# Kernel tuning notes

Hardware: AMD Instinct MI355X
Metric: run time of the kernel (lower is better)

The kernel has to match this reference:

```python
import jax, jax.numpy as jnp
import numpy as np

SEQ = 256  # position axis length fixed by the graph's iota(256)


def _mod(freq, phase):
    # sin(2*pi*t*freq + phase)^2 * 0.1 + 1 - 0.05, shape [SEQ]
    t = jnp.arange(SEQ, dtype=jnp.float32)
    return jnp.sin(t * (2.0 * jnp.pi) * freq + phase) ** 2 * 0.1 + 0.95


def setup_inputs() -> dict:
    key = jax.random.key(0)
    ks = jax.random.split(key, 16)
    K = 2048  # number of scattered index triples
    return {
        "primals_1": jax.random.normal(ks[0], (6, 256, 256), jnp.float32),
        "primals_2": jax.random.normal(ks[1], (12, 6, 256), jnp.float32),
        "primals_3": jax.random.normal(ks[2], (6, 256, 256), jnp.float32),
        "primals_4": jax.random.normal(ks[3], (6, 256), jnp.float32),
        "primals_5": jax.random.randint(ks[4], (K,), 0, 6),
        "primals_6": jax.random.randint(ks[5], (K,), 0, 256),
        "primals_7": jax.random.randint(ks[6], (K,), 0, 256),
        "primals_8": jax.random.randint(ks[7], (K,), 0, 256),
        "primals_9": jax.random.uniform(ks[8], (1,), jnp.float32),
        "primals_10": jax.random.uniform(ks[9], (1,), jnp.float32),
        "primals_11": jax.random.normal(ks[10], (6, 256), jnp.float32),
        "primals_12": jax.random.uniform(ks[11], (1,), jnp.float32),
        "primals_13": jax.random.uniform(ks[12], (1,), jnp.float32),
        "primals_14": jax.random.normal(ks[13], (6, 256), jnp.float32),
        "primals_15": jax.random.uniform(ks[14], (1,), jnp.float32),
        "primals_16": jax.random.uniform(ks[15], (1,), jnp.float32),
    }


def reference(primals_1, primals_2, primals_3, primals_4, primals_5, primals_6,
              primals_7, primals_8, primals_9, primals_10, primals_11, primals_12,
              primals_13, primals_14, primals_15, primals_16):
    decay = primals_3 * 0.975  # reused in all three stages

    def stage(q, table, freq, phase):
        # gather from table [6,256] at (p5,p6) -> [K]
        vals = table[primals_5, primals_6]
        # scatter into a fresh copy of the persistent buffer, then decay-accumulate
        mem = primals_1.at[primals_5, primals_7, primals_8].set(vals) + decay  # [6,256,256]
        # bmm 'attention': q [12,6,256] x mem [6,256,256] -> [12,6,256]
        att = jnp.einsum('hbd,bde->hbe', q, mem)
        return att, _mod(freq, phase)

    a1, m1 = stage(primals_2, primals_4, primals_9, primals_10)
    x1 = a1 / m1
    a2, m2 = stage(x1, primals_11, primals_12, primals_13)
    x2 = a2 * m2
    a3, m3 = stage(x2, primals_14, primals_15, primals_16)
    return a3 / m3
```

## Files before the change

kernel.cpp:

```cpp
#include <hip/hip_runtime.h>

#define TWO_PI 6.2831853071795864769f

__global__ __launch_bounds__(1024, 4) void fused_chain(
    const float* __restrict__ P1, const float* __restrict__ P2,
    const float* __restrict__ P3, const float* __restrict__ T4,
    const int* __restrict__ p5, const int* __restrict__ p6,
    const int* __restrict__ p7, const int* __restrict__ p8,
    const float* __restrict__ f1, const float* __restrict__ ph1,
    const float* __restrict__ T11, const float* __restrict__ f2,
    const float* __restrict__ ph2, const float* __restrict__ T14,
    const float* __restrict__ f3, const float* __restrict__ ph3,
    float* __restrict__ out, int K)
{
    __shared__ float v[256];
    __shared__ float pv[16][256];
    __shared__ float modl[3][256];
    __shared__ unsigned hmap[4096];
    __shared__ unsigned short wde[2048];
    __shared__ float wv0[2048], wv1[2048], wv2[2048];
    __shared__ int nw;

    const int blk = blockIdx.x;
    const int h = blk / 6;
    const int b = blk - h * 6;
    const int tid = (int)threadIdx.x;
    const int dg = tid >> 6;
    const int eg = tid & 63;

    const float4* P1v = (const float4*)P1;
    const float4* P3v = (const float4*)P3;
    const int rbase = (b << 8) + (dg << 4);
    float4 m4[16];
    #pragma unroll
    for (int i = 0; i < 16; ++i) {
        float4 a = P1v[(rbase + i) * 64 + eg];
        float4 c = P3v[(rbase + i) * 64 + eg];
        m4[i].x = fmaf(c.x, 0.975f, a.x);
        m4[i].y = fmaf(c.y, 0.975f, a.y);
        m4[i].z = fmaf(c.z, 0.975f, a.z);
        m4[i].w = fmaf(c.w, 0.975f, a.w);
    }

    if (tid < 256) v[tid] = P2[(h * 6 + b) * 256 + tid];
    if (tid < 768) {
        int s = tid >> 8, ee = tid & 255;
        float fr = (s == 0) ? f1[0]  : (s == 1) ? f2[0]  : f3[0];
        float ph = (s == 0) ? ph1[0] : (s == 1) ? ph2[0] : ph3[0];
        float sn = sinf((float)ee * TWO_PI * fr + ph);
        float mm = sn * sn * 0.1f + 0.95f;
        modl[s][ee] = (s == 1) ? mm : 1.0f / mm;
    }
    for (int i = tid; i < 4096; i += 1024) hmap[i] = 0xFFFFFFFFu;
    if (tid == 0) nw = 0;
    __syncthreads();

    for (int k = tid; k < K; k += 1024) {
        if (p5[k] != b) continue;
        unsigned key = ((unsigned)p7[k] << 8) | (unsigned)p8[k];
        unsigned mine = (key << 12) | (unsigned)k;
        unsigned hh = (key * 2654435761u) >> 20;
        for (;;) {
            unsigned prev = atomicCAS(&hmap[hh], 0xFFFFFFFFu, mine);
            if (prev == 0xFFFFFFFFu) break;
            if ((prev >> 12) == key) { atomicMax(&hmap[hh], mine); break; }
            hh = (hh + 1) & 4095u;
        }
    }
    __syncthreads();

    for (int k = tid; k < K; k += 1024) {
        if (p5[k] != b) continue;
        unsigned key = ((unsigned)p7[k] << 8) | (unsigned)p8[k];
        unsigned hh = (key * 2654435761u) >> 20;
        unsigned cur;
        for (;;) {
            cur = hmap[hh];
            if ((cur >> 12) == key) break;
            hh = (hh + 1) & 4095u;
        }
        if ((cur & 0xFFFu) == (unsigned)k) {
            int c = p6[k];
            float p1v = P1[(b << 16) | key];
            int w = atomicAdd(&nw, 1);
            wde[w] = (unsigned short)key;
            wv0[w] = T4 [b * 256 + c] - p1v;
            wv1[w] = T11[b * 256 + c] - p1v;
            wv2[w] = T14[b * 256 + c] - p1v;
        }
    }
    __syncthreads();
    const int nwl = nw;

    const int e256 = tid & 255;
    for (int s = 0; s < 3; ++s) {
        float4 acc = make_float4(0.f, 0.f, 0.f, 0.f);
        #pragma unroll
        for (int j = 0; j < 4; ++j) {
            float4 vv = *(const float4*)&v[(dg << 4) + (j << 2)];
            float4 m0 = m4[(j << 2) + 0];
            float4 m1 = m4[(j << 2) + 1];
            float4 m2 = m4[(j << 2) + 2];
            float4 m3 = m4[(j << 2) + 3];
            acc.x = fmaf(vv.x, m0.x, acc.x); acc.y = fmaf(vv.x, m0.y, acc.y);
            acc.z = fmaf(vv.x, m0.z, acc.z); acc.w = fmaf(vv.x, m0.w, acc.w);
            acc.x = fmaf(vv.y, m1.x, acc.x); acc.y = fmaf(vv.y, m1.y, acc.y);
            acc.z = fmaf(vv.y, m1.z, acc.z); acc.w = fmaf(vv.y, m1.w, acc.w);
            acc.x = fmaf(vv.z, m2.x, acc.x); acc.y = fmaf(vv.z, m2.y, acc.y);
            acc.z = fmaf(vv.z, m2.z, acc.z); acc.w = fmaf(vv.z, m2.w, acc.w);
            acc.x = fmaf(vv.w, m3.x, acc.x); acc.y = fmaf(vv.w, m3.y, acc.y);
            acc.z = fmaf(vv.w, m3.z, acc.z); acc.w = fmaf(vv.w, m3.w, acc.w);
        }
        *(float4*)&pv[dg][eg << 2] = acc;
        __syncthreads();
        {
            int r = tid >> 8;
            float x = pv[r][e256] + pv[r + 4][e256] +
                      pv[r + 8][e256] + pv[r + 12][e256];
            __syncthreads();
            pv[r][e256] = x;
        }
        __syncthreads();
        if (tid < 256)
            pv[0][tid] = (pv[0][tid] + pv[1][tid]) + (pv[2][tid] + pv[3][tid]);
        __syncthreads();
        const float* wvs = (s == 0) ? wv0 : (s == 1) ? wv1 : wv2;
        for (int i = tid; i < nwl; i += 1024) {
            unsigned de = wde[i];
            atomicAdd(&pv[0][de & 255u], v[de >> 8] * wvs[i]);
        }
        __syncthreads();
        if (tid < 256)
            v[tid] = pv[0][tid] * modl[s][tid];
        __syncthreads();
    }
    if (tid < 256) out[(h * 6 + b) * 256 + tid] = v[tid];
}

extern "C" void kernel_launch(void* const* d_in, const int* in_sizes, int n_in,
                              void* d_out, int out_size, void* d_ws, size_t ws_size,
                              hipStream_t stream)
{
    (void)n_in; (void)out_size; (void)d_ws; (void)ws_size;
    const float* P1  = (const float*)d_in[0];
    const float* P2  = (const float*)d_in[1];
    const float* P3  = (const float*)d_in[2];
    const float* T4  = (const float*)d_in[3];
    const int*   p5  = (const int*)d_in[4];
    const int*   p6  = (const int*)d_in[5];
    const int*   p7  = (const int*)d_in[6];
    const int*   p8  = (const int*)d_in[7];
    const float* f1  = (const float*)d_in[8];
    const float* ph1 = (const float*)d_in[9];
    const float* T11 = (const float*)d_in[10];
    const float* f2  = (const float*)d_in[11];
    const float* ph2 = (const float*)d_in[12];
    const float* T14 = (const float*)d_in[13];
    const float* f3  = (const float*)d_in[14];
    const float* ph3 = (const float*)d_in[15];
    float* out = (float*)d_out;
    int K = in_sizes[4];

    hipLaunchKernelGGL(fused_chain, dim3(72), dim3(1024), 0, stream,
                       P1, P2, P3, T4, p5, p6, p7, p8,
                       f1, ph1, T11, f2, ph2, T14, f3, ph3, out, K);
}
```

Baseline: 22.67 us.

## Split scatter dedup and decay precompute into a separate prep kernel

```diff
diff --git a/kernel.cpp b/kernel.cpp
--- a/kernel.cpp
+++ b/kernel.cpp
@@ -2,47 +2,107 @@
 
 #define TWO_PI 6.2831853071795864769f
 
-__global__ __launch_bounds__(1024, 4) void fused_chain(
-    const float* __restrict__ P1, const float* __restrict__ P2,
-    const float* __restrict__ P3, const float* __restrict__ T4,
+
+__global__ __launch_bounds__(1024) void prep_kernel(
+    const float* __restrict__ P1, const float* __restrict__ P3,
     const int* __restrict__ p5, const int* __restrict__ p6,
     const int* __restrict__ p7, const int* __restrict__ p8,
+    const float* __restrict__ T4, const float* __restrict__ T11,
+    const float* __restrict__ T14,
+    float* __restrict__ C, int* __restrict__ cnt,
+    int* __restrict__ wde_g, float* __restrict__ wv_g, int K)
+{
+    const int tid = (int)threadIdx.x;
+    const int blk = (int)blockIdx.x;
+    if (blk < 96) {
+        int i = blk * 1024 + tid;
+        float4 a = ((const float4*)P1)[i];
+        float4 c = ((const float4*)P3)[i];
+        float4 r;
+        r.x = fmaf(c.x, 0.975f, a.x);
+        r.y = fmaf(c.y, 0.975f, a.y);
+        r.z = fmaf(c.z, 0.975f, a.z);
+        r.w = fmaf(c.w, 0.975f, a.w);
+        ((float4*)C)[i] = r;
+        return;
+    }
+
+    __shared__ unsigned pk[2048];
+    __shared__ unsigned hmap[4096];
+    __shared__ int scnt[8];
+    for (int k = tid; k < K; k += 1024)
+        pk[k] = ((unsigned)p5[k] << 24) | ((unsigned)p6[k] << 16) |
+                ((unsigned)p7[k] << 8) | (unsigned)p8[k];
+    for (int i = tid; i < 4096; i += 1024) hmap[i] = 0xFFFFFFFFu;
+    if (tid < 8) scnt[tid] = 0;
+    __syncthreads();
+
+    for (int k = tid; k < K; k += 1024) {
+        unsigned v = pk[k];
+        unsigned key  = v & 0xFFFFu;
+        unsigned full = (key << 3) | (v >> 24);
+        unsigned mine = (full << 12) | (unsigned)k;
+        unsigned hh = (full * 2654435761u) >> 20;
+        for (;;) {
+            unsigned prev = atomicCAS(&hmap[hh], 0xFFFFFFFFu, mine);
+            if (prev == 0xFFFFFFFFu) break;
+            if ((prev >> 12) == full) { atomicMax(&hmap[hh], mine); break; }
+            hh = (hh + 1) & 4095u;
+        }
+    }
+    __syncthreads();
+
+    for (int k = tid; k < K; k += 1024) {
+        unsigned v = pk[k];
+        unsigned key  = v & 0xFFFFu;
+        unsigned full = (key << 3) | (v >> 24);
+        unsigned hh = (full * 2654435761u) >> 20;
+        unsigned cur;
+        for (;;) {
+            cur = hmap[hh];
+            if ((cur >> 12) == full) break;
+            hh = (hh + 1) & 4095u;
+        }
+        if ((cur & 0xFFFu) == (unsigned)k) {
+            int b = (int)(v >> 24), c = (int)((v >> 16) & 0xFFu);
+            float p1v = P1[(b << 16) | key];
+            int w = atomicAdd(&scnt[b], 1);
+            wde_g[b * 2048 + w] = (int)key;
+            wv_g[(0 * 6 + b) * 2048 + w] = T4 [b * 256 + c] - p1v;
+            wv_g[(1 * 6 + b) * 2048 + w] = T11[b * 256 + c] - p1v;
+            wv_g[(2 * 6 + b) * 2048 + w] = T14[b * 256 + c] - p1v;
+        }
+    }
+    __syncthreads();
+    if (tid < 8) cnt[tid] = scnt[tid];
+}
+
+__global__ __launch_bounds__(1024, 4) void chain_kernel(
+    const float* __restrict__ C, const float* __restrict__ P2,
+    const int* __restrict__ cnt, const int* __restrict__ wde_g,
+    const float* __restrict__ wv_g,
     const float* __restrict__ f1, const float* __restrict__ ph1,
-    const float* __restrict__ T11, const float* __restrict__ f2,
-    const float* __restrict__ ph2, const float* __restrict__ T14,
+    const float* __restrict__ f2, const float* __restrict__ ph2,
     const float* __restrict__ f3, const float* __restrict__ ph3,
-    float* __restrict__ out, int K)
+    float* __restrict__ out)
 {
-    __shared__ float v[256];
+    __shared__ float vbuf[2][256];
     __shared__ float pv[16][256];
     __shared__ float modl[3][256];
-    __shared__ unsigned hmap[4096];
-    __shared__ unsigned short wde[2048];
-    __shared__ float wv0[2048], wv1[2048], wv2[2048];
-    __shared__ int nw;
-
-    const int blk = blockIdx.x;
-    const int h = blk / 6;
-    const int b = blk - h * 6;
+    __shared__ int   wde[2048];
+    __shared__ float wvs[3][2048];
+
+    const int blk = (int)blockIdx.x;
+    const int h = blk / 6, b = blk - h * 6;
     const int tid = (int)threadIdx.x;
-    const int dg = tid >> 6;
-    const int eg = tid & 63;
-
-    const float4* P1v = (const float4*)P1;
-    const float4* P3v = (const float4*)P3;
-    const int rbase = (b << 8) + (dg << 4);
+    const int dg = tid >> 6, eg = tid & 63;
+
+    const float4* Cv = (const float4*)C + (((b << 8) + (dg << 4)) << 6) + eg;
     float4 m4[16];
     #pragma unroll
-    for (int i = 0; i < 16; ++i) {
-        float4 a = P1v[(rbase + i) * 64 + eg];
-        float4 c = P3v[(rbase + i) * 64 + eg];
-        m4[i].x = fmaf(c.x, 0.975f, a.x);
-        m4[i].y = fmaf(c.y, 0.975f, a.y);
-        m4[i].z = fmaf(c.z, 0.975f, a.z);
-        m4[i].w = fmaf(c.w, 0.975f, a.w);
-    }
-
-    if (tid < 256) v[tid] = P2[(h * 6 + b) * 256 + tid];
+    for (int i = 0; i < 16; ++i) m4[i] = Cv[i << 6];
+
+    if (tid < 256) vbuf[0][tid] = P2[(h * 6 + b) * 256 + tid];
     if (tid < 768) {
         int s = tid >> 8, ee = tid & 255;
         float fr = (s == 0) ? f1[0]  : (s == 1) ? f2[0]  : f3[0];
@@ -51,53 +111,23 @@
         float mm = sn * sn * 0.1f + 0.95f;
         modl[s][ee] = (s == 1) ? mm : 1.0f / mm;
     }
-    for (int i = tid; i < 4096; i += 1024) hmap[i] = 0xFFFFFFFFu;
-    if (tid == 0) nw = 0;
-    __syncthreads();
-
-    for (int k = tid; k < K; k += 1024) {
-        if (p5[k] != b) continue;
-        unsigned key = ((unsigned)p7[k] << 8) | (unsigned)p8[k];
-        unsigned mine = (key << 12) | (unsigned)k;
-        unsigned hh = (key * 2654435761u) >> 20;
-        for (;;) {
-            unsigned prev = atomicCAS(&hmap[hh], 0xFFFFFFFFu, mine);
-            if (prev == 0xFFFFFFFFu) break;
-            if ((prev >> 12) == key) { atomicMax(&hmap[hh], mine); break; }
-            hh = (hh + 1) & 4095u;
-        }
-    }
-    __syncthreads();
-
-    for (int k = tid; k < K; k += 1024) {
-        if (p5[k] != b) continue;
-        unsigned key = ((unsigned)p7[k] << 8) | (unsigned)p8[k];
-        unsigned hh = (key * 2654435761u) >> 20;
-        unsigned cur;
-        for (;;) {
-            cur = hmap[hh];
-            if ((cur >> 12) == key) break;
-            hh = (hh + 1) & 4095u;
-        }
-        if ((cur & 0xFFFu) == (unsigned)k) {
-            int c = p6[k];
-            float p1v = P1[(b << 16) | key];
-            int w = atomicAdd(&nw, 1);
-            wde[w] = (unsigned short)key;
-            wv0[w] = T4 [b * 256 + c] - p1v;
-            wv1[w] = T11[b * 256 + c] - p1v;
-            wv2[w] = T14[b * 256 + c] - p1v;
-        }
-    }
-    __syncthreads();
-    const int nwl = nw;
-
-    const int e256 = tid & 255;
+    const int nwl = cnt[b];
+    for (int i = tid; i < nwl; i += 1024) {
+        wde[i]    = wde_g[b * 2048 + i];
+        wvs[0][i] = wv_g[(0 * 6 + b) * 2048 + i];
+        wvs[1][i] = wv_g[(1 * 6 + b) * 2048 + i];
+        wvs[2][i] = wv_g[(2 * 6 + b) * 2048 + i];
+    }
+    __syncthreads();
+
+    int cur = 0;
     for (int s = 0; s < 3; ++s) {
+        const float* vin = vbuf[cur];
+        float* vout = vbuf[cur ^ 1];
         float4 acc = make_float4(0.f, 0.f, 0.f, 0.f);
         #pragma unroll
         for (int j = 0; j < 4; ++j) {
-            float4 vv = *(const float4*)&v[(dg << 4) + (j << 2)];
+            float4 vv = *(const float4*)&vin[(dg << 4) + (j << 2)];
             float4 m0 = m4[(j << 2) + 0];
             float4 m1 = m4[(j << 2) + 1];
             float4 m2 = m4[(j << 2) + 2];
@@ -113,35 +143,29 @@
         }
         *(float4*)&pv[dg][eg << 2] = acc;
         __syncthreads();
-        {
-            int r = tid >> 8;
-            float x = pv[r][e256] + pv[r + 4][e256] +
-                      pv[r + 8][e256] + pv[r + 12][e256];
-            __syncthreads();
-            pv[r][e256] = x;
+        if (tid < 256) {
+            float x = 0.f;
+            #pragma unroll
+            for (int r = 0; r < 16; ++r) x += pv[r][tid];
+            vout[tid] = x * modl[s][tid];
         }
         __syncthreads();
-        if (tid < 256)
-            pv[0][tid] = (pv[0][tid] + pv[1][tid]) + (pv[2][tid] + pv[3][tid]);
+        for (int i = tid; i < nwl; i += 1024) {
+            int de = wde[i];
+            atomicAdd(&vout[de & 255],
+                      vin[de >> 8] * wvs[s][i] * modl[s][de & 255]);
+        }
         __syncthreads();
-        const float* wvs = (s == 0) ? wv0 : (s == 1) ? wv1 : wv2;
-        for (int i = tid; i < nwl; i += 1024) {
-            unsigned de = wde[i];
-            atomicAdd(&pv[0][de & 255u], v[de >> 8] * wvs[i]);
-        }
-        __syncthreads();
-        if (tid < 256)
-            v[tid] = pv[0][tid] * modl[s][tid];
-        __syncthreads();
-    }
-    if (tid < 256) out[(h * 6 + b) * 256 + tid] = v[tid];
+        cur ^= 1;
+    }
+    if (tid < 256) out[(h * 6 + b) * 256 + tid] = vbuf[cur][tid];
 }
 
 extern "C" void kernel_launch(void* const* d_in, const int* in_sizes, int n_in,
                               void* d_out, int out_size, void* d_ws, size_t ws_size,
                               hipStream_t stream)
 {
-    (void)n_in; (void)out_size; (void)d_ws; (void)ws_size;
+    (void)n_in; (void)out_size; (void)ws_size;
     const float* P1  = (const float*)d_in[0];
     const float* P2  = (const float*)d_in[1];
     const float* P3  = (const float*)d_in[2];
@@ -161,7 +185,16 @@
     float* out = (float*)d_out;
     int K = in_sizes[4];
 
-    hipLaunchKernelGGL(fused_chain, dim3(72), dim3(1024), 0, stream,
-                       P1, P2, P3, T4, p5, p6, p7, p8,
-                       f1, ph1, T11, f2, ph2, T14, f3, ph3, out, K);
+    char* ws = (char*)d_ws;
+    float* C     = (float*)(ws);
+    int*   cnt   = (int*)  (ws + 1572864);
+    int*   wde_g = (int*)  (ws + 1572928);
+    float* wv_g  = (float*)(ws + 1622080);
+
+    hipLaunchKernelGGL(prep_kernel, dim3(97), dim3(1024), 0, stream,
+                       P1, P3, p5, p6, p7, p8, T4, T11, T14,
+                       C, cnt, wde_g, wv_g, K);
+    hipLaunchKernelGGL(chain_kernel, dim3(72), dim3(1024), 0, stream,
+                       C, P2, cnt, wde_g, wv_g,
+                       f1, ph1, f2, ph2, f3, ph3, out);
 }
```

Result: slower. 23.61 us (+4.1%).
